# Optimization experiments

Hardware: AMD Instinct MI355X
Metric: run time of the kernel (lower is better)

## Reference

```python
import jax, jax.numpy as jnp
import numpy as np

HEADS = 8
DIM_HEAD = 128
BUCKET_SIZE = 128


def setup_inputs() -> dict:
    key = jax.random.key(0)
    ks = jax.random.split(key, 5)
    b, t, d = 4, 4096, 1024
    dh_all = HEADS * DIM_HEAD  # 1024
    x = jax.random.normal(ks[0], (b, t, d), dtype=jnp.float32)
    # 0.02 init scale keeps qk logits in a sane range (mimics trained-weight scale)
    Wq = jax.random.normal(ks[1], (d, dh_all), dtype=jnp.float32) * 0.02
    Wkv = jax.random.normal(ks[2], (d, 2 * dh_all), dtype=jnp.float32) * 0.02
    Wo = jax.random.normal(ks[3], (dh_all, d), dtype=jnp.float32) * 0.02
    bo = jnp.zeros((d,), dtype=jnp.float32)
    return {"x": x, "Wq": Wq, "Wkv": Wkv, "Wo": Wo, "bo": bo}


def reference(x, Wq, Wkv, Wo, bo):
    b, t, d = x.shape
    h, dh, bs = HEADS, DIM_HEAD, BUCKET_SIZE
    buckets = t // bs
    scale = dh ** -0.5

    # projections (Linear without bias for q/kv)
    q = x @ Wq                      # [b, t, h*dh]
    k, v = jnp.split(x @ Wkv, 2, axis=-1)

    def merge_heads(u):             # [b, t, h*dh] -> [b*h, t, dh]
        return u.reshape(b, t, h, dh).transpose(0, 2, 1, 3).reshape(b * h, t, dh)

    q, k, v = merge_heads(q), merge_heads(k), merge_heads(v)

    # bucket: [b*h, buckets, bs, dh]
    bq = q.reshape(b * h, buckets, bs, dh)
    bk = k.reshape(b * h, buckets, bs, dh)
    bv = v.reshape(b * h, buckets, bs, dh)

    # AttentionSortNet (non_permutative=True): bucket-mean similarity -> softmax
    sq = bq.mean(axis=2)            # [b*h, buckets, dh]
    sk = bk.mean(axis=2)
    R = jnp.einsum('bie,bje->bij', sq, sk) * scale
    R = jax.nn.softmax(R, axis=-1)  # [b*h, buckets, buckets]

    # soft-reorder kv buckets and concat with local buckets (n_sortcut == 0)
    bk_r = jnp.einsum('buv,bvtd->butd', R, bk)
    bv_r = jnp.einsum('buv,bvtd->butd', R, bv)
    bk_cat = jnp.concatenate([bk_r, bk], axis=2)   # [b*h, buckets, 2*bs, dh]
    bv_cat = jnp.concatenate([bv_r, bv], axis=2)

    # per-bucket attention
    dots = jnp.einsum('buie,buje->buij', bq, bk_cat) * scale
    attn = jax.nn.softmax(dots, axis=-1)
    out = jnp.einsum('buij,buje->buie', attn, bv_cat)  # [b*h, buckets, bs, dh]

    # unbucket + split heads back: [b, t, h*dh]
    out = out.reshape(b, h, t, dh).transpose(0, 2, 1, 3).reshape(b, t, h * dh)
    return out @ Wo + bo
```

## Files before the change

### kernel.cpp

```cpp
#include <hip/hip_runtime.h>
#include <hip/hip_bf16.h>
#include <stdint.h>

typedef short short8 __attribute__((ext_vector_type(8)));
typedef float f32x4 __attribute__((ext_vector_type(4)));
typedef float f32x2 __attribute__((ext_vector_type(2)));

__device__ __forceinline__ unsigned short f2bf(float f) {
    unsigned u = __float_as_uint(f);
    u += 0x7fff + ((u >> 16) & 1);
    return (unsigned short)(u >> 16);
}
__device__ __forceinline__ float bf2f(unsigned short h) {
    return __uint_as_float(((unsigned)h) << 16);
}

__device__ __forceinline__ void gload_lds16(const void* g, void* l) {
    __builtin_amdgcn_global_load_lds(
        (const __attribute__((address_space(1))) void*)g,
        (__attribute__((address_space(3))) void*)l, 16, 0, 0);
}

__global__ void cast_x_kernel(const float* __restrict__ x, unsigned short* __restrict__ xb, int n) {
    int i = (blockIdx.x * blockDim.x + threadIdx.x) * 4;
    int stride = gridDim.x * blockDim.x * 4;
    for (; i < n; i += stride) {
        float4 f = *(const float4*)(x + i);
        ushort4 o;
        o.x = f2bf(f.x); o.y = f2bf(f.y); o.z = f2bf(f.z); o.w = f2bf(f.w);
        *(ushort4*)(xb + i) = o;
    }
}

__global__ void transpose_cast_kernel(const float* __restrict__ W, unsigned short* __restrict__ Wt,
                                      int K, int N) {
    __shared__ unsigned short tile[32][33];
    int k0 = blockIdx.x * 32, n0 = blockIdx.y * 32;
    int tx = threadIdx.x & 31, ty = threadIdx.x >> 5;
#pragma unroll
    for (int i = 0; i < 32; i += 8)
        tile[ty + i][tx] = f2bf(W[(size_t)(k0 + ty + i) * N + n0 + tx]);
    __syncthreads();
#pragma unroll
    for (int i = 0; i < 32; i += 8)
        Wt[(size_t)(n0 + ty + i) * K + k0 + tx] = tile[tx][ty + i];
}

__global__ __launch_bounds__(512, 4)
void gemmQKV(const unsigned short* __restrict__ A, const unsigned short* __restrict__ B,
             unsigned short* __restrict__ qb, unsigned short* __restrict__ kb,
             unsigned short* __restrict__ vtb, float* __restrict__ sq, float* __restrict__ sk) {
    __shared__ unsigned short Ssh[65536];
    const int tid = threadIdx.x;
    const int w = tid >> 6, lane = tid & 63;
    const int lr = lane & 15, lg = lane >> 4, r7 = lane & 7;
    const int wr = w >> 2, wc = w & 3;
    const int orig = blockIdx.x;
    const int lgc = (orig & 7) * 96 + (orig >> 3);
    const int m0 = (lgc / 12) * 256;
    const int p = lgc % 12;
    const int nG = p * 256;
    const int mode = p >> 2;
    const int n0 = (p & 3) * 256;
    const int srow8 = lane >> 3;
    const int sgrp = (lane & 7) ^ srow8;
    const unsigned short* gA = A + (size_t)(m0 + w * 16 + srow8) * 1024 + sgrp * 8;
    const unsigned short* gB = B + (size_t)(nG + w * 16 + srow8) * 1024 + sgrp * 8;

    f32x4 acc[8][4] = {};

#define SH(BUF, HALF, KT) {                                                              \
        const unsigned short* gp_ = ((HALF) < 2 ? gA : gB) +                             \
                                    (size_t)(((HALF) & 1) * 128) * 1024 + (KT);          \
        unsigned short* lp_ = Ssh + ((HALF) < 2 ? 0 : 32768) + (BUF) * 16384 +           \
                              ((HALF) & 1) * 8192 + w * 1024;                            \
        gload_lds16(gp_, lp_);                                                           \
        gload_lds16(gp_ + 8192, lp_ + 512);                                              \
    }

    SH(0, 0, 0) SH(0, 1, 0) SH(0, 2, 0) SH(0, 3, 0)
    SH(1, 0, 64) SH(1, 1, 64) SH(1, 2, 64)
    asm volatile("s_waitcnt vmcnt(6)" ::: "memory");
    __builtin_amdgcn_sched_barrier(0);
    __builtin_amdgcn_s_barrier();

#pragma unroll 2
    for (int t = 0; t < 16; ++t) {
        const int cur = t & 1;
        const unsigned short* Ab = Ssh + cur * 16384;
        const unsigned short* Bb = Ssh + 32768 + cur * 16384;
        const int kt1 = (t + 1) * 64, kt2 = (t + 2) * 64;
        short8 af[8][2], bf[4][2];

#pragma unroll
        for (int mi = 0; mi < 4; ++mi)
#pragma unroll
            for (int kk = 0; kk < 2; ++kk)
                af[mi][kk] = *(const short8*)(Ab + (wr * 128 + mi * 16 + lr) * 64 +
                                              (((kk << 2) | lg) ^ r7) * 8);
#pragma unroll
        for (int ni = 0; ni < 2; ++ni)
#pragma unroll
            for (int kk = 0; kk < 2; ++kk)
                bf[ni][kk] = *(const short8*)(Bb + (wc * 64 + ni * 16 + lr) * 64 +
                                              (((kk << 2) | lg) ^ r7) * 8);
        if (t + 1 < 16) { SH(cur ^ 1, 3, kt1) }
        asm volatile("s_waitcnt lgkmcnt(8)" ::: "memory");
        __builtin_amdgcn_sched_barrier(0);
        __builtin_amdgcn_s_barrier();
        asm volatile("s_waitcnt lgkmcnt(0)" ::: "memory");
        __builtin_amdgcn_sched_barrier(0);
        __builtin_amdgcn_s_setprio(1);
#pragma unroll
        for (int mi = 0; mi < 4; ++mi)
#pragma unroll
            for (int ni = 0; ni < 2; ++ni)
#pragma unroll
                for (int kk = 0; kk < 2; ++kk)
                    acc[mi][ni] = __builtin_amdgcn_mfma_f32_16x16x32_bf16(af[mi][kk], bf[ni][kk],
                                                                          acc[mi][ni], 0, 0, 0);
        __builtin_amdgcn_s_setprio(0);
        __builtin_amdgcn_s_barrier();

#pragma unroll
        for (int mi = 4; mi < 8; ++mi)
#pragma unroll
            for (int kk = 0; kk < 2; ++kk)
                af[mi][kk] = *(const short8*)(Ab + (wr * 128 + mi * 16 + lr) * 64 +
                                              (((kk << 2) | lg) ^ r7) * 8);
        if (t + 2 < 16) { SH(cur, 0, kt2) }
        __builtin_amdgcn_s_barrier();
        asm volatile("s_waitcnt lgkmcnt(0)" ::: "memory");
        __builtin_amdgcn_sched_barrier(0);
        __builtin_amdgcn_s_setprio(1);
#pragma unroll
        for (int mi = 4; mi < 8; ++mi)
#pragma unroll
            for (int ni = 0; ni < 2; ++ni)
#pragma unroll
                for (int kk = 0; kk < 2; ++kk)
                    acc[mi][ni] = __builtin_amdgcn_mfma_f32_16x16x32_bf16(af[mi][kk], bf[ni][kk],
                                                                          acc[mi][ni], 0, 0, 0);
        __builtin_amdgcn_s_setprio(0);
        __builtin_amdgcn_s_barrier();

#pragma unroll
        for (int ni = 2; ni < 4; ++ni)
#pragma unroll
            for (int kk = 0; kk < 2; ++kk)
                bf[ni][kk] = *(const short8*)(Bb + (wc * 64 + ni * 16 + lr) * 64 +
                                              (((kk << 2) | lg) ^ r7) * 8);
        if (t + 2 < 16) { SH(cur, 1, kt2) }
        __builtin_amdgcn_s_barrier();
        asm volatile("s_waitcnt lgkmcnt(0)" ::: "memory");
        __builtin_amdgcn_sched_barrier(0);
        __builtin_amdgcn_s_setprio(1);
#pragma unroll
        for (int mi = 4; mi < 8; ++mi)
#pragma unroll
            for (int ni = 2; ni < 4; ++ni)
#pragma unroll
                for (int kk = 0; kk < 2; ++kk)
                    acc[mi][ni] = __builtin_amdgcn_mfma_f32_16x16x32_bf16(af[mi][kk], bf[ni][kk],
                                                                          acc[mi][ni], 0, 0, 0);
        __builtin_amdgcn_s_setprio(0);
        __builtin_amdgcn_s_barrier();

        if (t + 2 < 16) { SH(cur, 2, kt2) }
        __builtin_amdgcn_s_setprio(1);
#pragma unroll
        for (int mi = 0; mi < 4; ++mi)
#pragma unroll
            for (int ni = 2; ni < 4; ++ni)
#pragma unroll
                for (int kk = 0; kk < 2; ++kk)
                    acc[mi][ni] = __builtin_amdgcn_mfma_f32_16x16x32_bf16(af[mi][kk], bf[ni][kk],
                                                                          acc[mi][ni], 0, 0, 0);
        __builtin_amdgcn_s_setprio(0);
        if (t < 14) {
            asm volatile("s_waitcnt vmcnt(6)" ::: "memory");
            __builtin_amdgcn_sched_barrier(0);
            __builtin_amdgcn_s_barrier();
        } else if (t == 14) {
            asm volatile("s_waitcnt vmcnt(0)" ::: "memory");
            __builtin_amdgcn_sched_barrier(0);
            __builtin_amdgcn_s_barrier();
        }
    }
#undef SH

    if (mode == 2) {
#pragma unroll
        for (int mi = 0; mi < 8; ++mi)
#pragma unroll
            for (int ni = 0; ni < 4; ++ni) {
                int gm0 = m0 + wr * 128 + mi * 16 + lg * 4;
                int gn = n0 + wc * 64 + ni * 16 + lr;
                int b = gm0 >> 12, tt0 = gm0 & 4095, h = gn >> 7, dl = gn & 127;
                int u = tt0 >> 7, tl0 = tt0 & 127;
                size_t base = (size_t)(b * 8 + h) * 524288 + (size_t)u * 16384 + dl * 128 + tl0;
#pragma unroll
                for (int r = 0; r < 4; r += 2) {
                    unsigned pk = (unsigned)f2bf(acc[mi][ni][r]) |
                                  ((unsigned)f2bf(acc[mi][ni][r + 1]) << 16);
                    *(unsigned*)(vtb + base + r) = pk;
                }
            }
    } else {
        unsigned short* obf = (mode == 0) ? qb : kb;
        const float osc = (mode == 0) ? 0.08838834764831845f : 1.0f;
#pragma unroll
        for (int mi = 0; mi < 8; ++mi)
#pragma unroll
            for (int ni = 0; ni < 4; ++ni)
#pragma unroll
                for (int r = 0; r < 4; ++r) {
                    int gm = m0 + wr * 128 + mi * 16 + lg * 4 + r;
                    int gn = n0 + wc * 64 + ni * 16 + lr;
                    int b = gm >> 12, tt = gm & 4095, h = gn >> 7, dl = gn & 127;
                    obf[(size_t)(b * 8 + h) * 524288 + (size_t)tt * 128 + dl] =
                        f2bf(acc[mi][ni][r] * osc);
                }
        float* of = (mode == 0) ? sq : sk;
        const float sc = ((mode == 0) ? 0.08838834764831845f : 1.0f) / 128.f;
#pragma unroll
        for (int ni = 0; ni < 4; ++ni) {
            float ssum = 0.f;
#pragma unroll
            for (int mi = 0; mi < 8; ++mi)
#pragma unroll
                for (int r = 0; r < 4; ++r) ssum += acc[mi][ni][r];
            ssum += __shfl_xor(ssum, 16);
            ssum += __shfl_xor(ssum, 32);
            if (lane < 16) {
                int gn = n0 + wc * 64 + ni * 16 + lr;
                int h = gn >> 7, dl = gn & 127;
                int bh = (m0 >> 12) * 8 + h;
                int u = ((m0 & 4095) >> 7) + wr;
                of[(size_t)(bh * 32 + u) * 128 + dl] = ssum * sc;
            }
        }
    }
}

__global__ __launch_bounds__(512, 2)
void gemmOut(const unsigned short* __restrict__ A, const unsigned short* __restrict__ B,
             float* __restrict__ of, const float* __restrict__ bias) {
    __shared__ unsigned short Ssh[65536];
    const int tid = threadIdx.x;
    const int w = tid >> 6, lane = tid & 63;
    const int lr = lane & 15, lg = lane >> 4, r7 = lane & 7;
    const int wr = w >> 2, wc = w & 3;
    const int orig = blockIdx.x;
    const int lgc = (orig & 7) * 32 + (orig >> 3);
    const int m0 = (lgc >> 2) * 256, n0 = (lgc & 3) * 256;
    const int srow8 = lane >> 3;
    const int sgrp = (lane & 7) ^ srow8;
    const unsigned short* gA = A + (size_t)(m0 + w * 16 + srow8) * 1024 + sgrp * 8;
    const unsigned short* gB = B + (size_t)(n0 + w * 16 + srow8) * 1024 + sgrp * 8;

    f32x4 acc[8][4] = {};

#define SH(BUF, HALF, KT) {                                                              \
        const unsigned short* gp_ = ((HALF) < 2 ? gA : gB) +                             \
                                    (size_t)(((HALF) & 1) * 128) * 1024 + (KT);          \
        unsigned short* lp_ = Ssh + ((HALF) < 2 ? 0 : 32768) + (BUF) * 16384 +           \
                              ((HALF) & 1) * 8192 + w * 1024;                            \
        gload_lds16(gp_, lp_);                                                           \
        gload_lds16(gp_ + 8192, lp_ + 512);                                              \
    }

    SH(0, 0, 0) SH(0, 1, 0) SH(0, 2, 0) SH(0, 3, 0)
    SH(1, 0, 64) SH(1, 1, 64) SH(1, 2, 64)
    asm volatile("s_waitcnt vmcnt(6)" ::: "memory");
    __builtin_amdgcn_sched_barrier(0);
    __builtin_amdgcn_s_barrier();

#pragma unroll 2
    for (int t = 0; t < 16; ++t) {
        const int cur = t & 1;
        const unsigned short* Ab = Ssh + cur * 16384;
        const unsigned short* Bb = Ssh + 32768 + cur * 16384;
        const int kt1 = (t + 1) * 64, kt2 = (t + 2) * 64;
        short8 af[8][2], bf[4][2];

#pragma unroll
        for (int mi = 0; mi < 4; ++mi)
#pragma unroll
            for (int kk = 0; kk < 2; ++kk)
                af[mi][kk] = *(const short8*)(Ab + (wr * 128 + mi * 16 + lr) * 64 +
                                              (((kk << 2) | lg) ^ r7) * 8);
#pragma unroll
        for (int ni = 0; ni < 2; ++ni)
#pragma unroll
            for (int kk = 0; kk < 2; ++kk)
                bf[ni][kk] = *(const short8*)(Bb + (wc * 64 + ni * 16 + lr) * 64 +
                                              (((kk << 2) | lg) ^ r7) * 8);
        if (t + 1 < 16) { SH(cur ^ 1, 3, kt1) }
        asm volatile("s_waitcnt lgkmcnt(8)" ::: "memory");
        __builtin_amdgcn_sched_barrier(0);
        __builtin_amdgcn_s_barrier();
        asm volatile("s_waitcnt lgkmcnt(0)" ::: "memory");
        __builtin_amdgcn_sched_barrier(0);
        __builtin_amdgcn_s_setprio(1);
#pragma unroll
        for (int mi = 0; mi < 4; ++mi)
#pragma unroll
            for (int ni = 0; ni < 2; ++ni)
#pragma unroll
                for (int kk = 0; kk < 2; ++kk)
                    acc[mi][ni] = __builtin_amdgcn_mfma_f32_16x16x32_bf16(af[mi][kk], bf[ni][kk],
                                                                          acc[mi][ni], 0, 0, 0);
        __builtin_amdgcn_s_setprio(0);
        __builtin_amdgcn_s_barrier();

#pragma unroll
        for (int mi = 4; mi < 8; ++mi)
#pragma unroll
            for (int kk = 0; kk < 2; ++kk)
                af[mi][kk] = *(const short8*)(Ab + (wr * 128 + mi * 16 + lr) * 64 +
                                              (((kk << 2) | lg) ^ r7) * 8);
        if (t + 2 < 16) { SH(cur, 0, kt2) }
        __builtin_amdgcn_s_barrier();
        asm volatile("s_waitcnt lgkmcnt(0)" ::: "memory");
        __builtin_amdgcn_sched_barrier(0);
        __builtin_amdgcn_s_setprio(1);
#pragma unroll
        for (int mi = 4; mi < 8; ++mi)
#pragma unroll
            for (int ni = 0; ni < 2; ++ni)
#pragma unroll
                for (int kk = 0; kk < 2; ++kk)
                    acc[mi][ni] = __builtin_amdgcn_mfma_f32_16x16x32_bf16(af[mi][kk], bf[ni][kk],
                                                                          acc[mi][ni], 0, 0, 0);
        __builtin_amdgcn_s_setprio(0);
        __builtin_amdgcn_s_barrier();

#pragma unroll
        for (int ni = 2; ni < 4; ++ni)
#pragma unroll
            for (int kk = 0; kk < 2; ++kk)
                bf[ni][kk] = *(const short8*)(Bb + (wc * 64 + ni * 16 + lr) * 64 +
                                              (((kk << 2) | lg) ^ r7) * 8);
        if (t + 2 < 16) { SH(cur, 1, kt2) }
        __builtin_amdgcn_s_barrier();
        asm volatile("s_waitcnt lgkmcnt(0)" ::: "memory");
        __builtin_amdgcn_sched_barrier(0);
        __builtin_amdgcn_s_setprio(1);
#pragma unroll
        for (int mi = 4; mi < 8; ++mi)
#pragma unroll
            for (int ni = 2; ni < 4; ++ni)
#pragma unroll
                for (int kk = 0; kk < 2; ++kk)
                    acc[mi][ni] = __builtin_amdgcn_mfma_f32_16x16x32_bf16(af[mi][kk], bf[ni][kk],
                                                                          acc[mi][ni], 0, 0, 0);
        __builtin_amdgcn_s_setprio(0);
        __builtin_amdgcn_s_barrier();

        if (t + 2 < 16) { SH(cur, 2, kt2) }
        __builtin_amdgcn_s_setprio(1);
#pragma unroll
        for (int mi = 0; mi < 4; ++mi)
#pragma unroll
            for (int ni = 2; ni < 4; ++ni)
#pragma unroll
                for (int kk = 0; kk < 2; ++kk)
                    acc[mi][ni] = __builtin_amdgcn_mfma_f32_16x16x32_bf16(af[mi][kk], bf[ni][kk],
                                                                          acc[mi][ni], 0, 0, 0);
        __builtin_amdgcn_s_setprio(0);
        if (t < 14) {
            asm volatile("s_waitcnt vmcnt(6)" ::: "memory");
            __builtin_amdgcn_sched_barrier(0);
            __builtin_amdgcn_s_barrier();
        } else if (t == 14) {
            asm volatile("s_waitcnt vmcnt(0)" ::: "memory");
            __builtin_amdgcn_sched_barrier(0);
            __builtin_amdgcn_s_barrier();
        }
    }
#undef SH

#pragma unroll
    for (int mi = 0; mi < 8; ++mi)
#pragma unroll
        for (int ni = 0; ni < 4; ++ni)
#pragma unroll
            for (int r = 0; r < 4; ++r) {
                int gm = m0 + wr * 128 + mi * 16 + lg * 4 + r;
                int gn = n0 + wc * 64 + ni * 16 + lr;
                of[(size_t)gm * 1024 + gn] = acc[mi][ni][r] + bias[gn];
            }
}

__global__ void sortnet_kernel(const float* __restrict__ sq, const float* __restrict__ sk,
                               float* __restrict__ R) {
    __shared__ float qs[32 * 129];
    __shared__ float ks[32 * 129];
    int bh = blockIdx.x, tid = threadIdx.x;
    for (int i = tid; i < 4096; i += 1024) {
        int row = i >> 7, col = i & 127;
        qs[row * 129 + col] = sq[(size_t)bh * 4096 + i];
        ks[row * 129 + col] = sk[(size_t)bh * 4096 + i];
    }
    __syncthreads();
    int u = tid >> 5, v = tid & 31;
    float dot = 0.f;
    for (int d = 0; d < 128; ++d) dot += qs[u * 129 + d] * ks[v * 129 + d];
    float mx = dot;
    for (int m = 16; m >= 1; m >>= 1) mx = fmaxf(mx, __shfl_xor(mx, m, 32));
    float e = __expf(dot - mx);
    float s = e;
    for (int m = 16; m >= 1; m >>= 1) s += __shfl_xor(s, m, 32);
    R[(size_t)bh * 1024 + u * 32 + v] = e / s;
}

__global__ __launch_bounds__(256, 4)
void mix_kernel(const unsigned short* __restrict__ k, const unsigned short* __restrict__ vT,
                const float* __restrict__ R, unsigned short* __restrict__ bkr,
                unsigned short* __restrict__ bvrT) {
    const int bid = blockIdx.x;
    const int arr = bid & 1;
    const int rest = bid >> 1;
    const int bh = rest >> 5, chunk = rest & 31;
    const int tid = threadIdx.x;
    const unsigned short* __restrict__ src = arr ? vT : k;
    unsigned short* __restrict__ dst = arr ? bvrT : bkr;
    const float* __restrict__ Rb = R + (size_t)bh * 1024;

    const int e = chunk * 512 + tid * 2;
    const size_t base = (size_t)bh * 524288 + e;

    unsigned raw[32];
#pragma unroll
    for (int vb = 0; vb < 32; ++vb)
        raw[vb] = *(const unsigned*)(src + base + (size_t)vb * 16384);
    f32x2 val[32];
#pragma unroll
    for (int vb = 0; vb < 32; ++vb)
        val[vb] = f32x2{bf2f((unsigned short)raw[vb]), bf2f((unsigned short)(raw[vb] >> 16))};

#pragma unroll 2
    for (int u = 0; u < 32; ++u) {
        f32x2 a0 = {0.f, 0.f}, a1 = {0.f, 0.f}, a2 = {0.f, 0.f}, a3 = {0.f, 0.f};
#pragma unroll
        for (int g = 0; g < 2; ++g) {
            float4 r0 = *(const float4*)(Rb + u * 32 + g * 16);
            float4 r1 = *(const float4*)(Rb + u * 32 + g * 16 + 4);
            float4 r2 = *(const float4*)(Rb + u * 32 + g * 16 + 8);
            float4 r3 = *(const float4*)(Rb + u * 32 + g * 16 + 12);
            const int b0 = g * 16;
            a0 += r0.x * val[b0 + 0];  a0 += r0.y * val[b0 + 1];
            a0 += r0.z * val[b0 + 2];  a0 += r0.w * val[b0 + 3];
            a1 += r1.x * val[b0 + 4];  a1 += r1.y * val[b0 + 5];
            a1 += r1.z * val[b0 + 6];  a1 += r1.w * val[b0 + 7];
            a2 += r2.x * val[b0 + 8];  a2 += r2.y * val[b0 + 9];
            a2 += r2.z * val[b0 + 10]; a2 += r2.w * val[b0 + 11];
            a3 += r3.x * val[b0 + 12]; a3 += r3.y * val[b0 + 13];
            a3 += r3.z * val[b0 + 14]; a3 += r3.w * val[b0 + 15];
        }
        f32x2 a = (a0 + a1) + (a2 + a3);
        unsigned o = (unsigned)f2bf(a.x) | ((unsigned)f2bf(a.y) << 16);
        *(unsigned*)(dst + (size_t)bh * 524288 + (size_t)u * 16384 + e) = o;
    }
}

__global__ __launch_bounds__(512)
void attn_kernel(const unsigned short* __restrict__ q, const unsigned short* __restrict__ k,
                 const unsigned short* __restrict__ vT, const unsigned short* __restrict__ bkr,
                 const unsigned short* __restrict__ bvrT, unsigned short* __restrict__ ao) {
    __shared__ unsigned short KB[2][8192];
    __shared__ unsigned short VB[2][8192];
    __shared__ unsigned short Ps[8][1024];
    const int orig = blockIdx.x;
    const int bid = (orig & 7) * 128 + (orig >> 3);
    const int bh = bid >> 5, u = bid & 31;
    const int tid = threadIdx.x, w = tid >> 6, lane = tid & 63;
    const int lr = lane & 15, lg = lane >> 4;
    const size_t bb = (size_t)bh * 524288 + (size_t)u * 16384;

#define STAGE_K(SRC, BUF)                                                        \
    _Pragma("unroll")                                                            \
    for (int i = 0; i < 2; ++i) {                                                \
        const int row_ = i * 32 + (tid >> 4);                                    \
        gload_lds16((SRC) + row_ * 128 + (((tid & 15) ^ (row_ & 7)) * 8),        \
                    (char*)KB[BUF] + i * 8192 + tid * 16);                       \
    }
#define STAGE_V(SRC, BUF)                                                        \
    _Pragma("unroll")                                                            \
    for (int i = 0; i < 2; ++i) {                                                \
        const int row_ = i * 64 + (tid >> 3);                                    \
        gload_lds16((SRC) + row_ * 128 + (((tid & 7) ^ (row_ & 7)) * 8),         \
                    (char*)VB[BUF] + i * 8192 + tid * 16);                       \
    }

    const unsigned short* qg = q + bb + (size_t)(w * 16) * 128;
    short8 aq[4];
#pragma unroll
    for (int kk = 0; kk < 4; ++kk)
        aq[kk] = *(const short8*)(qg + lr * 128 + kk * 32 + lg * 8);

    STAGE_K(bkr + bb, 0) STAGE_V(bvrT + bb, 0)
    STAGE_K(bkr + bb + 8192, 1) STAGE_V(bvrT + bb + 64, 1)

    short8 ones8;
#pragma unroll
    for (int i = 0; i < 8; ++i) ones8[i] = (short)0x3F80;

    f32x4 oacc[8] = {};
    f32x4 lacc = {};

    asm volatile("s_waitcnt vmcnt(4)" ::: "memory");
    __builtin_amdgcn_sched_barrier(0);
    __builtin_amdgcn_s_barrier();

    unsigned short* Pw = Ps[w];

#pragma unroll
    for (int c = 0; c < 4; ++c) {
        const int cb = c & 1;
        f32x4 s[4] = {};
        __builtin_amdgcn_s_setprio(1);
#pragma unroll
        for (int kk = 0; kk < 4; ++kk)
#pragma unroll
            for (int ni = 0; ni < 4; ++ni) {
                short8 kb8 = *(const short8*)(&KB[cb][(ni * 16 + lr) * 128 +
                                              (((kk * 4 + lg) ^ (lr & 7)) * 8)]);
                s[ni] = __builtin_amdgcn_mfma_f32_16x16x32_bf16(aq[kk], kb8, s[ni], 0, 0, 0);
            }
        __builtin_amdgcn_s_setprio(0);

#pragma unroll
        for (int r = 0; r < 4; ++r) {
            int prow = lg * 4 + r;
#pragma unroll
            for (int ni = 0; ni < 4; ++ni)
                Pw[prow * 64 + ((ni * 16 + lr) ^ ((prow & 7) << 3))] = f2bf(__expf(s[ni][r]));
        }

        __builtin_amdgcn_s_setprio(1);
#pragma unroll
        for (int ks2 = 0; ks2 < 2; ++ks2) {
            short8 ap = *(const short8*)(&Pw[lr * 64 + ((ks2 * 32 + lg * 8) ^ ((lr & 7) << 3))]);
            lacc = __builtin_amdgcn_mfma_f32_16x16x32_bf16(ap, ones8, lacc, 0, 0, 0);
#pragma unroll
            for (int ni = 0; ni < 8; ++ni) {
                short8 bv8 = *(const short8*)(&VB[cb][(ni * 16 + lr) * 64 +
                                              (((ks2 * 4 + lg) ^ (lr & 7)) * 8)]);
                oacc[ni] = __builtin_amdgcn_mfma_f32_16x16x32_bf16(ap, bv8, oacc[ni], 0, 0, 0);
            }
        }
        __builtin_amdgcn_s_setprio(0);

        __builtin_amdgcn_s_barrier();
        if (c == 0) { STAGE_K(k + bb, 0) STAGE_V(vT + bb, 0) }
        else if (c == 1) { STAGE_K(k + bb + 8192, 1) STAGE_V(vT + bb + 64, 1) }
        if (c < 2) {
            asm volatile("s_waitcnt vmcnt(4)" ::: "memory");
            __builtin_amdgcn_sched_barrier(0);
            __builtin_amdgcn_s_barrier();
        } else if (c == 2) {
            asm volatile("s_waitcnt vmcnt(0)" ::: "memory");
            __builtin_amdgcn_sched_barrier(0);
            __builtin_amdgcn_s_barrier();
        }
    }

    const int b = bh >> 3, h = bh & 7;
#pragma unroll
    for (int r = 0; r < 4; ++r) {
        int row = w * 16 + lg * 4 + r;
        size_t rowbase = ((size_t)b * 4096 + u * 128 + row) * 1024 + h * 128;
        float inv = 1.f / lacc[r];
#pragma unroll
        for (int ni = 0; ni < 8; ++ni)
            ao[rowbase + ni * 16 + lr] = f2bf(oacc[ni][r] * inv);
    }
#undef STAGE_K
#undef STAGE_V
}

extern "C" void kernel_launch(void* const* d_in, const int* in_sizes, int n_in,
                              void* d_out, int out_size, void* d_ws, size_t ws_size,
                              hipStream_t stream) {
    (void)in_sizes; (void)n_in; (void)out_size; (void)ws_size;
    const float* x   = (const float*)d_in[0];
    const float* Wq  = (const float*)d_in[1];
    const float* Wkv = (const float*)d_in[2];
    const float* Wo  = (const float*)d_in[3];
    const float* bo  = (const float*)d_in[4];
    float* out = (float*)d_out;

    char* ws = (char*)d_ws;
    const size_t SZ_BIG = 33554432;
    unsigned short* xb    = (unsigned short*)(ws);
    unsigned short* qb    = (unsigned short*)(ws + SZ_BIG);
    unsigned short* kb    = (unsigned short*)(ws + 2 * SZ_BIG);
    unsigned short* vtb   = (unsigned short*)(ws + 3 * SZ_BIG);
    unsigned short* bkr   = (unsigned short*)(ws + 4 * SZ_BIG);
    unsigned short* bvrT  = (unsigned short*)(ws + 5 * SZ_BIG);
    size_t off = 6 * SZ_BIG;
    unsigned short* wqkvt = (unsigned short*)(ws + off); off += 6291456;
    unsigned short* wot   = (unsigned short*)(ws + off); off += 2097152;
    float* sq   = (float*)(ws + off); off += 524288;
    float* sk   = (float*)(ws + off); off += 524288;
    float* Rbuf = (float*)(ws + off); off += 131072;

    cast_x_kernel<<<4096, 256, 0, stream>>>(x, xb, 16777216);
    transpose_cast_kernel<<<dim3(32, 32), 256, 0, stream>>>(Wq, wqkvt, 1024, 1024);
    transpose_cast_kernel<<<dim3(32, 64), 256, 0, stream>>>(Wkv, wqkvt + 1048576, 1024, 2048);
    transpose_cast_kernel<<<dim3(32, 32), 256, 0, stream>>>(Wo, wot, 1024, 1024);

    gemmQKV<<<768, 512, 0, stream>>>(xb, wqkvt, qb, kb, vtb, sq, sk);

    sortnet_kernel<<<32, 1024, 0, stream>>>(sq, sk, Rbuf);
    mix_kernel<<<2048, 256, 0, stream>>>(kb, vtb, Rbuf, bkr, bvrT);

    attn_kernel<<<1024, 512, 0, stream>>>(qb, kb, vtb, bkr, bvrT, xb);

    gemmOut<<<256, 512, 0, stream>>>(xb, wot, out, bo);
}
```

Baseline: 257.7 us.

## Make QKV GEMM persistent over three N-tiles with continuous prefetch pipeline

The QKV projection GEMM now launches 256 blocks instead of 768, and each block computes three consecutive 256-wide output tiles for the same M rows. The global-to-LDS prefetch pipeline runs continuously across the three tiles, so the pipeline fill and drain cost is paid once per block rather than once per tile. Between tiles the epilogue runs and the accumulators are reset. The trade-off is that exactly 256 blocks leaves less tail balancing across CUs, and the epilogue stores are now serialized between tiles inside each block.

```diff
diff --git a/kernel.cpp b/kernel.cpp
--- a/kernel.cpp
+++ b/kernel.cpp
@@ -56,191 +56,202 @@
     const int lr = lane & 15, lg = lane >> 4, r7 = lane & 7;
     const int wr = w >> 2, wc = w & 3;
     const int orig = blockIdx.x;
-    const int lgc = (orig & 7) * 96 + (orig >> 3);
-    const int m0 = (lgc / 12) * 256;
-    const int p = lgc % 12;
-    const int nG = p * 256;
-    const int mode = p >> 2;
-    const int n0 = (p & 3) * 256;
+    const int lgc = (orig & 7) * 32 + (orig >> 3);
+    const int m0 = (lgc >> 2) * 256;
+    const int p0 = (lgc & 3) * 3;
     const int srow8 = lane >> 3;
     const int sgrp = (lane & 7) ^ srow8;
     const unsigned short* gA = A + (size_t)(m0 + w * 16 + srow8) * 1024 + sgrp * 8;
-    const unsigned short* gB = B + (size_t)(nG + w * 16 + srow8) * 1024 + sgrp * 8;
+    const unsigned short* gB = B + (size_t)(p0 * 256 + w * 16 + srow8) * 1024 + sgrp * 8;
 
     f32x4 acc[8][4] = {};
 
-#define SH(BUF, HALF, KT) {                                                              \
-        const unsigned short* gp_ = ((HALF) < 2 ? gA : gB) +                             \
-                                    (size_t)(((HALF) & 1) * 128) * 1024 + (KT);          \
-        unsigned short* lp_ = Ssh + ((HALF) < 2 ? 0 : 32768) + (BUF) * 16384 +           \
+#define SH(HALF, ST) {                                                                   \
+        const int t_ = (ST) >> 4, k_ = ((ST) & 15) * 64;                                 \
+        const unsigned short* gp_ = ((HALF) < 2 ? gA : gB + (size_t)t_ * 262144) +       \
+                                    (size_t)(((HALF) & 1) * 128) * 1024 + k_;            \
+        unsigned short* lp_ = Ssh + ((HALF) < 2 ? 0 : 32768) + ((ST) & 1) * 16384 +      \
                               ((HALF) & 1) * 8192 + w * 1024;                            \
         gload_lds16(gp_, lp_);                                                           \
         gload_lds16(gp_ + 8192, lp_ + 512);                                              \
     }
 
-    SH(0, 0, 0) SH(0, 1, 0) SH(0, 2, 0) SH(0, 3, 0)
-    SH(1, 0, 64) SH(1, 1, 64) SH(1, 2, 64)
+    SH(0, 0) SH(1, 0) SH(2, 0) SH(3, 0)
+    SH(0, 1) SH(1, 1) SH(2, 1)
     asm volatile("s_waitcnt vmcnt(6)" ::: "memory");
     __builtin_amdgcn_sched_barrier(0);
     __builtin_amdgcn_s_barrier();
 
+    for (int seg = 0; seg < 3; ++seg) {
+        const int p = p0 + seg;
+        const int mode = p >> 2;
+        const int n0 = (p & 3) * 256;
+
 #pragma unroll 2
-    for (int t = 0; t < 16; ++t) {
-        const int cur = t & 1;
-        const unsigned short* Ab = Ssh + cur * 16384;
-        const unsigned short* Bb = Ssh + 32768 + cur * 16384;
-        const int kt1 = (t + 1) * 64, kt2 = (t + 2) * 64;
-        short8 af[8][2], bf[4][2];
-
-#pragma unroll
-        for (int mi = 0; mi < 4; ++mi)
-#pragma unroll
-            for (int kk = 0; kk < 2; ++kk)
-                af[mi][kk] = *(const short8*)(Ab + (wr * 128 + mi * 16 + lr) * 64 +
-                                              (((kk << 2) | lg) ^ r7) * 8);
-#pragma unroll
-        for (int ni = 0; ni < 2; ++ni)
-#pragma unroll
-            for (int kk = 0; kk < 2; ++kk)
-                bf[ni][kk] = *(const short8*)(Bb + (wc * 64 + ni * 16 + lr) * 64 +
-                                              (((kk << 2) | lg) ^ r7) * 8);
-        if (t + 1 < 16) { SH(cur ^ 1, 3, kt1) }
-        asm volatile("s_waitcnt lgkmcnt(8)" ::: "memory");
-        __builtin_amdgcn_sched_barrier(0);
-        __builtin_amdgcn_s_barrier();
-        asm volatile("s_waitcnt lgkmcnt(0)" ::: "memory");
-        __builtin_amdgcn_sched_barrier(0);
-        __builtin_amdgcn_s_setprio(1);
-#pragma unroll
-        for (int mi = 0; mi < 4; ++mi)
+        for (int t = 0; t < 16; ++t) {
+            const int gs = (seg << 4) | t;
+            const int cur = gs & 1;
+            const unsigned short* Ab = Ssh + cur * 16384;
+            const unsigned short* Bb = Ssh + 32768 + cur * 16384;
+            short8 af[8][2], bf[4][2];
+
+#pragma unroll
+            for (int mi = 0; mi < 4; ++mi)
+#pragma unroll
+                for (int kk = 0; kk < 2; ++kk)
+                    af[mi][kk] = *(const short8*)(Ab + (wr * 128 + mi * 16 + lr) * 64 +
+                                                  (((kk << 2) | lg) ^ r7) * 8);
 #pragma unroll
             for (int ni = 0; ni < 2; ++ni)
 #pragma unroll
                 for (int kk = 0; kk < 2; ++kk)
-                    acc[mi][ni] = __builtin_amdgcn_mfma_f32_16x16x32_bf16(af[mi][kk], bf[ni][kk],
-                                                                          acc[mi][ni], 0, 0, 0);
-        __builtin_amdgcn_s_setprio(0);
-        __builtin_amdgcn_s_barrier();
-
-#pragma unroll
-        for (int mi = 4; mi < 8; ++mi)
-#pragma unroll
-            for (int kk = 0; kk < 2; ++kk)
-                af[mi][kk] = *(const short8*)(Ab + (wr * 128 + mi * 16 + lr) * 64 +
-                                              (((kk << 2) | lg) ^ r7) * 8);
-        if (t + 2 < 16) { SH(cur, 0, kt2) }
-        __builtin_amdgcn_s_barrier();
-        asm volatile("s_waitcnt lgkmcnt(0)" ::: "memory");
-        __builtin_amdgcn_sched_barrier(0);
-        __builtin_amdgcn_s_setprio(1);
-#pragma unroll
-        for (int mi = 4; mi < 8; ++mi)
-#pragma unroll
-            for (int ni = 0; ni < 2; ++ni)
-#pragma unroll
-                for (int kk = 0; kk < 2; ++kk)
-                    acc[mi][ni] = __builtin_amdgcn_mfma_f32_16x16x32_bf16(af[mi][kk], bf[ni][kk],
-                                                                          acc[mi][ni], 0, 0, 0);
-        __builtin_amdgcn_s_setprio(0);
-        __builtin_amdgcn_s_barrier();
-
-#pragma unroll
-        for (int ni = 2; ni < 4; ++ni)
-#pragma unroll
-            for (int kk = 0; kk < 2; ++kk)
-                bf[ni][kk] = *(const short8*)(Bb + (wc * 64 + ni * 16 + lr) * 64 +
-                                              (((kk << 2) | lg) ^ r7) * 8);
-        if (t + 2 < 16) { SH(cur, 1, kt2) }
-        __builtin_amdgcn_s_barrier();
-        asm volatile("s_waitcnt lgkmcnt(0)" ::: "memory");
-        __builtin_amdgcn_sched_barrier(0);
-        __builtin_amdgcn_s_setprio(1);
-#pragma unroll
-        for (int mi = 4; mi < 8; ++mi)
+                    bf[ni][kk] = *(const short8*)(Bb + (wc * 64 + ni * 16 + lr) * 64 +
+                                                  (((kk << 2) | lg) ^ r7) * 8);
+            if (gs + 1 < 48) { SH(3, gs + 1) }
+            asm volatile("s_waitcnt lgkmcnt(8)" ::: "memory");
+            __builtin_amdgcn_sched_barrier(0);
+            __builtin_amdgcn_s_barrier();
+            asm volatile("s_waitcnt lgkmcnt(0)" ::: "memory");
+            __builtin_amdgcn_sched_barrier(0);
+            __builtin_amdgcn_s_setprio(1);
+#pragma unroll
+            for (int mi = 0; mi < 4; ++mi)
+#pragma unroll
+                for (int ni = 0; ni < 2; ++ni)
+#pragma unroll
+                    for (int kk = 0; kk < 2; ++kk)
+                        acc[mi][ni] = __builtin_amdgcn_mfma_f32_16x16x32_bf16(
+                            af[mi][kk], bf[ni][kk], acc[mi][ni], 0, 0, 0);
+            __builtin_amdgcn_s_setprio(0);
+            __builtin_amdgcn_s_barrier();
+
+#pragma unroll
+            for (int mi = 4; mi < 8; ++mi)
+#pragma unroll
+                for (int kk = 0; kk < 2; ++kk)
+                    af[mi][kk] = *(const short8*)(Ab + (wr * 128 + mi * 16 + lr) * 64 +
+                                                  (((kk << 2) | lg) ^ r7) * 8);
+            if (gs + 2 < 48) { SH(0, gs + 2) }
+            __builtin_amdgcn_s_barrier();
+            asm volatile("s_waitcnt lgkmcnt(0)" ::: "memory");
+            __builtin_amdgcn_sched_barrier(0);
+            __builtin_amdgcn_s_setprio(1);
+#pragma unroll
+            for (int mi = 4; mi < 8; ++mi)
+#pragma unroll
+                for (int ni = 0; ni < 2; ++ni)
+#pragma unroll
+                    for (int kk = 0; kk < 2; ++kk)
+                        acc[mi][ni] = __builtin_amdgcn_mfma_f32_16x16x32_bf16(
+                            af[mi][kk], bf[ni][kk], acc[mi][ni], 0, 0, 0);
+            __builtin_amdgcn_s_setprio(0);
+            __builtin_amdgcn_s_barrier();
+
 #pragma unroll
             for (int ni = 2; ni < 4; ++ni)
 #pragma unroll
                 for (int kk = 0; kk < 2; ++kk)
-                    acc[mi][ni] = __builtin_amdgcn_mfma_f32_16x16x32_bf16(af[mi][kk], bf[ni][kk],
-                                                                          acc[mi][ni], 0, 0, 0);
-        __builtin_amdgcn_s_setprio(0);
-        __builtin_amdgcn_s_barrier();
-
-        if (t + 2 < 16) { SH(cur, 2, kt2) }
-        __builtin_amdgcn_s_setprio(1);
-#pragma unroll
-        for (int mi = 0; mi < 4; ++mi)
-#pragma unroll
-            for (int ni = 2; ni < 4; ++ni)
-#pragma unroll
-                for (int kk = 0; kk < 2; ++kk)
-                    acc[mi][ni] = __builtin_amdgcn_mfma_f32_16x16x32_bf16(af[mi][kk], bf[ni][kk],
-                                                                          acc[mi][ni], 0, 0, 0);
-        __builtin_amdgcn_s_setprio(0);
-        if (t < 14) {
-            asm volatile("s_waitcnt vmcnt(6)" ::: "memory");
-            __builtin_amdgcn_sched_barrier(0);
-            __builtin_amdgcn_s_barrier();
-        } else if (t == 14) {
-            asm volatile("s_waitcnt vmcnt(0)" ::: "memory");
-            __builtin_amdgcn_sched_barrier(0);
-            __builtin_amdgcn_s_barrier();
+                    bf[ni][kk] = *(const short8*)(Bb + (wc * 64 + ni * 16 + lr) * 64 +
+                                                  (((kk << 2) | lg) ^ r7) * 8);
+            if (gs + 2 < 48) { SH(1, gs + 2) }
+            __builtin_amdgcn_s_barrier();
+            asm volatile("s_waitcnt lgkmcnt(0)" ::: "memory");
+            __builtin_amdgcn_sched_barrier(0);
+            __builtin_amdgcn_s_setprio(1);
+#pragma unroll
+            for (int mi = 4; mi < 8; ++mi)
+#pragma unroll
+                for (int ni = 2; ni < 4; ++ni)
+#pragma unroll
+                    for (int kk = 0; kk < 2; ++kk)
+                        acc[mi][ni] = __builtin_amdgcn_mfma_f32_16x16x32_bf16(
+                            af[mi][kk], bf[ni][kk], acc[mi][ni], 0, 0, 0);
+            __builtin_amdgcn_s_setprio(0);
+            __builtin_amdgcn_s_barrier();
+
+            if (gs + 2 < 48) { SH(2, gs + 2) }
+            __builtin_amdgcn_s_setprio(1);
+#pragma unroll
+            for (int mi = 0; mi < 4; ++mi)
+#pragma unroll
+                for (int ni = 2; ni < 4; ++ni)
+#pragma unroll
+                    for (int kk = 0; kk < 2; ++kk)
+                        acc[mi][ni] = __builtin_amdgcn_mfma_f32_16x16x32_bf16(
+                            af[mi][kk], bf[ni][kk], acc[mi][ni], 0, 0, 0);
+            __builtin_amdgcn_s_setprio(0);
+            if (gs < 46) {
+                asm volatile("s_waitcnt vmcnt(6)" ::: "memory");
+                __builtin_amdgcn_sched_barrier(0);
+                __builtin_amdgcn_s_barrier();
+            } else if (gs == 46) {
+                asm volatile("s_waitcnt vmcnt(0)" ::: "memory");
+                __builtin_amdgcn_sched_barrier(0);
+                __builtin_amdgcn_s_barrier();
+            }
         }
-    }
-#undef SH
-
-    if (mode == 2) {
-#pragma unroll
-        for (int mi = 0; mi < 8; ++mi)
+
+        if (mode == 2) {
+#pragma unroll
+            for (int mi = 0; mi < 8; ++mi)
+#pragma unroll
+                for (int ni = 0; ni < 4; ++ni) {
+                    int gm0 = m0 + wr * 128 + mi * 16 + lg * 4;
+                    int gn = n0 + wc * 64 + ni * 16 + lr;
+                    int b = gm0 >> 12, tt0 = gm0 & 4095, h = gn >> 7, dl = gn & 127;
+                    int u = tt0 >> 7, tl0 = tt0 & 127;
+                    size_t base = (size_t)(b * 8 + h) * 524288 + (size_t)u * 16384 +
+                                  dl * 128 + tl0;
+#pragma unroll
+                    for (int r = 0; r < 4; r += 2) {
+                        unsigned pk = (unsigned)f2bf(acc[mi][ni][r]) |
+                                      ((unsigned)f2bf(acc[mi][ni][r + 1]) << 16);
+                        *(unsigned*)(vtb + base + r) = pk;
+                    }
+                }
+        } else {
+            unsigned short* obf = (mode == 0) ? qb : kb;
+            const float osc = (mode == 0) ? 0.08838834764831845f : 1.0f;
+#pragma unroll
+            for (int mi = 0; mi < 8; ++mi)
+#pragma unroll
+                for (int ni = 0; ni < 4; ++ni)
+#pragma unroll
+                    for (int r = 0; r < 4; ++r) {
+                        int gm = m0 + wr * 128 + mi * 16 + lg * 4 + r;
+                        int gn = n0 + wc * 64 + ni * 16 + lr;
+                        int b = gm >> 12, tt = gm & 4095, h = gn >> 7, dl = gn & 127;
+                        obf[(size_t)(b * 8 + h) * 524288 + (size_t)tt * 128 + dl] =
+                            f2bf(acc[mi][ni][r] * osc);
+                    }
+            float* of = (mode == 0) ? sq : sk;
+            const float sc = ((mode == 0) ? 0.08838834764831845f : 1.0f) / 128.f;
 #pragma unroll
             for (int ni = 0; ni < 4; ++ni) {
-                int gm0 = m0 + wr * 128 + mi * 16 + lg * 4;
-                int gn = n0 + wc * 64 + ni * 16 + lr;
-                int b = gm0 >> 12, tt0 = gm0 & 4095, h = gn >> 7, dl = gn & 127;
-                int u = tt0 >> 7, tl0 = tt0 & 127;
-                size_t base = (size_t)(b * 8 + h) * 524288 + (size_t)u * 16384 + dl * 128 + tl0;
-#pragma unroll
-                for (int r = 0; r < 4; r += 2) {
-                    unsigned pk = (unsigned)f2bf(acc[mi][ni][r]) |
-                                  ((unsigned)f2bf(acc[mi][ni][r + 1]) << 16);
-                    *(unsigned*)(vtb + base + r) = pk;
+                float ssum = 0.f;
+#pragma unroll
+                for (int mi = 0; mi < 8; ++mi)
+#pragma unroll
+                    for (int r = 0; r < 4; ++r) ssum += acc[mi][ni][r];
+                ssum += __shfl_xor(ssum, 16);
+                ssum += __shfl_xor(ssum, 32);
+                if (lane < 16) {
+                    int gn = n0 + wc * 64 + ni * 16 + lr;
+                    int h = gn >> 7, dl = gn & 127;
+                    int bh = (m0 >> 12) * 8 + h;
+                    int u = ((m0 & 4095) >> 7) + wr;
+                    of[(size_t)(bh * 32 + u) * 128 + dl] = ssum * sc;
                 }
             }
-    } else {
-        unsigned short* obf = (mode == 0) ? qb : kb;
-        const float osc = (mode == 0) ? 0.08838834764831845f : 1.0f;
+        }
+
 #pragma unroll
         for (int mi = 0; mi < 8; ++mi)
 #pragma unroll
             for (int ni = 0; ni < 4; ++ni)
-#pragma unroll
-                for (int r = 0; r < 4; ++r) {
-                    int gm = m0 + wr * 128 + mi * 16 + lg * 4 + r;
-                    int gn = n0 + wc * 64 + ni * 16 + lr;
-                    int b = gm >> 12, tt = gm & 4095, h = gn >> 7, dl = gn & 127;
-                    obf[(size_t)(b * 8 + h) * 524288 + (size_t)tt * 128 + dl] =
-                        f2bf(acc[mi][ni][r] * osc);
-                }
-        float* of = (mode == 0) ? sq : sk;
-        const float sc = ((mode == 0) ? 0.08838834764831845f : 1.0f) / 128.f;
-#pragma unroll
-        for (int ni = 0; ni < 4; ++ni) {
-            float ssum = 0.f;
-#pragma unroll
-            for (int mi = 0; mi < 8; ++mi)
-#pragma unroll
-                for (int r = 0; r < 4; ++r) ssum += acc[mi][ni][r];
-            ssum += __shfl_xor(ssum, 16);
-            ssum += __shfl_xor(ssum, 32);
-            if (lane < 16) {
-                int gn = n0 + wc * 64 + ni * 16 + lr;
-                int h = gn >> 7, dl = gn & 127;
-                int bh = (m0 >> 12) * 8 + h;
-                int u = ((m0 & 4095) >> 7) + wr;
-                of[(size_t)(bh * 32 + u) * 128 + dl] = ssum * sc;
-            }
-        }
-    }
+                acc[mi][ni] = f32x4{0.f, 0.f, 0.f, 0.f};
+    }
+#undef SH
 }
 
 __global__ __launch_bounds__(512, 2)
@@ -612,7 +623,7 @@
     transpose_cast_kernel<<<dim3(32, 64), 256, 0, stream>>>(Wkv, wqkvt + 1048576, 1024, 2048);
     transpose_cast_kernel<<<dim3(32, 32), 256, 0, stream>>>(Wo, wot, 1024, 1024);
 
-    gemmQKV<<<768, 512, 0, stream>>>(xb, wqkvt, qb, kb, vtb, sq, sk);
+    gemmQKV<<<256, 512, 0, stream>>>(xb, wqkvt, qb, kb, vtb, sq, sk);
 
     sortnet_kernel<<<32, 1024, 0, stream>>>(sq, sk, Rbuf);
     mix_kernel<<<2048, 256, 0, stream>>>(kb, vtb, Rbuf, bkr, bvrT);
```

New measurement: 281.2 us. +9.1%, slower.
